# Performance work log

Measured on AMD Instinct MI355X. Metric: run time of the kernel, lower is better.

The kernel has to match this reference:

```python
import jax, jax.numpy as jnp
import numpy as np

W = 0.5  # loss weight from __init__
EPS = 1e-14


def gradient_l2_loss(x):
    """Mean squared forward finite-difference along each spatial axis of (B,s,r,c)."""
    loss = 0.0
    for ax in (1, 2, 3):
        d = jnp.diff(x, axis=ax)
        loss = loss + jnp.mean(d * d)
    return loss


def setup_inputs() -> dict:
    key = jax.random.key(0)
    k1, k2 = jax.random.split(key)
    B, S, R, C = 2, 128, 128, 128
    L = jax.random.normal(k1, (B, 3, S, R, C), dtype=jnp.float32)
    U = jax.random.normal(k2, (B, 9, S, R, C), dtype=jnp.float32)
    return {"L": L, "U": U}


def reference(L, U):
    B, _, S, R, C = U.shape
    # torch.sort(L, dim=1, descending=True) -> indices[:,0] == argmax over the 3 eigenvalues
    idx0 = jnp.argmax(L, axis=1)  # (B,S,R,C) int
    # U channel layout U{row}_{col}: reshape to (B, col=3, row=3, S,R,C)
    Uview = U.reshape(B, 3, 3, S, R, C)
    idx = jnp.broadcast_to(idx0[:, None, None], (B, 3, 1, S, R, C))
    # faithful to original gather(dim=2)[:, :, 0]
    major = jnp.take_along_axis(Uview, idx, axis=2)[:, :, 0]  # (B,3,S,R,C)
    am = jnp.abs(major)
    den = jnp.sum(am * am, axis=1)  # (B,S,R,C)
    den = jnp.where(den < EPS, EPS, den)
    e1, e2, e3 = am[:, 0], am[:, 1], am[:, 2]
    CO = jnp.sqrt(0.5 * ((e1 - e2) ** 2 + (e2 - e3) ** 2 + (e3 - e1) ** 2) / den)
    CO_grad = 0.0
    for i in range(9):  # fixed small channel loop
        CO_grad = CO_grad + gradient_l2_loss(U[:, i])
    return (CO + CO_grad).mean() * W
```

## Files before the change

### kernel.cpp

```cpp
#include <hip/hip_runtime.h>

#define SS 128
#define RR 128
#define CC 128
#define SCH 4
#define EPSF 1e-14f

__global__ __launch_bounds__(256, 4) void scol_main(const float* __restrict__ L,
                                                    const float* __restrict__ U,
                                                    float4* __restrict__ part) {
    const int SRC = SS * RR * CC;
    const int RC  = RR * CC;

    int bid = blockIdx.x;
    int cpx = gridDim.x >> 3;
    int swz = (bid & 7) * cpx + (bid >> 3);

    int rt = swz & 15;
    int sc = (swz >> 4) & 31;
    int b  = swz >> 9;

    int tid = threadIdx.x;
    int c4       = tid & 31;
    int rowLocal = tid >> 5;
    int r  = (rt << 3) + rowLocal;
    int s0 = sc * SCH;
    int c  = c4 << 2;

    bool hr = (r < RR - 1), hc = (c4 < 31);
    float wr = hr ? 1.f : 0.f;
    float wc = hc ? 1.f : 0.f;
    int offr = hr ? CC : 0;

    int pos = (s0 * RR + r) * CC + c;
    const float* Ub = U + (size_t)b * 9 * SRC + pos;
    const float* Lb = L + (size_t)b * 3 * SRC + pos;

    float a_dc = 0.f, a_dr = 0.f, a_ds = 0.f, a_co = 0.f;

    float4 prev[9];
#pragma unroll
    for (int ch = 0; ch < 9; ++ch)
        prev[ch] = *(const float4*)(Ub + ch * SRC);

#pragma unroll 1
    for (int ss = 0; ss < SCH; ++ss) {
        const float* Up = Ub + ss * RC;
        const float* Lp = Lb + ss * RC;

        float4 l0 = *(const float4*)(Lp);
        float4 l1 = *(const float4*)(Lp + SRC);
        float4 l2 = *(const float4*)(Lp + 2 * SRC);
        float L0v[4] = {l0.x, l0.y, l0.z, l0.w};
        float L1v[4] = {l1.x, l1.y, l1.z, l1.w};
        float L2v[4] = {l2.x, l2.y, l2.z, l2.w};
        int idx[4];
#pragma unroll
        for (int j = 0; j < 4; ++j) {
            int id = 0;
            float best = L0v[j];
            if (L1v[j] > best) { best = L1v[j]; id = 1; }
            if (L2v[j] > best) { best = L2v[j]; id = 2; }
            idx[j] = id;
        }

        float am[3][4];
#pragma unroll
        for (int g = 0; g < 3; ++g)
#pragma unroll
            for (int j = 0; j < 4; ++j) am[g][j] = 0.f;

        float t_dcb = 0.f, t_dr = 0.f;

#pragma unroll
        for (int ch = 0; ch < 9; ++ch) {
            float4 uu = *(const float4*)(Up + ch * SRC);
            float4 vr = *(const float4*)(Up + ch * SRC + offr);
            float4 pv = prev[ch];

            int g = ch / 3, m = ch % 3;
            float uuv[4] = {uu.x, uu.y, uu.z, uu.w};
#pragma unroll
            for (int j = 0; j < 4; ++j)
                if (idx[j] == m) am[g][j] = fabsf(uuv[j]);

            float d;
            d = uu.y - uu.x; a_dc += d * d;
            d = uu.z - uu.y; a_dc += d * d;
            d = uu.w - uu.z; a_dc += d * d;
            float un = __shfl_down(uu.x, 1);
            d = un - uu.w; t_dcb += d * d;

            d = vr.x - uu.x; t_dr += d * d;
            d = vr.y - uu.y; t_dr += d * d;
            d = vr.z - uu.z; t_dr += d * d;
            d = vr.w - uu.w; t_dr += d * d;

            d = uu.x - pv.x; a_ds += d * d;
            d = uu.y - pv.y; a_ds += d * d;
            d = uu.z - pv.z; a_ds += d * d;
            d = uu.w - pv.w; a_ds += d * d;

            prev[ch] = uu;
        }
        a_dc += wc * t_dcb;
        a_dr += wr * t_dr;

#pragma unroll
        for (int j = 0; j < 4; ++j) {
            float e1 = am[0][j], e2 = am[1][j], e3 = am[2][j];
            float den = e1 * e1 + e2 * e2 + e3 * e3;
            den = fmaxf(den, EPSF);
            float num = 0.5f * ((e1 - e2) * (e1 - e2) + (e2 - e3) * (e2 - e3) +
                                (e3 - e1) * (e3 - e1));
            a_co += sqrtf(num / den);
        }
    }

    if (s0 + SCH < SS) {
        const float* Up = Ub + SCH * RC;
#pragma unroll
        for (int ch = 0; ch < 9; ++ch) {
            float4 uu = *(const float4*)(Up + ch * SRC);
            float4 pv = prev[ch];
            float d;
            d = uu.x - pv.x; a_ds += d * d;
            d = uu.y - pv.y; a_ds += d * d;
            d = uu.z - pv.z; a_ds += d * d;
            d = uu.w - pv.w; a_ds += d * d;
        }
    }

#pragma unroll
    for (int off = 32; off > 0; off >>= 1) {
        a_co += __shfl_down(a_co, off);
        a_ds += __shfl_down(a_ds, off);
        a_dr += __shfl_down(a_dr, off);
        a_dc += __shfl_down(a_dc, off);
    }

    __shared__ float s_co[4], s_ds[4], s_dr[4], s_dc[4];
    int wid  = threadIdx.x >> 6;
    int lane = threadIdx.x & 63;
    if (lane == 0) {
        s_co[wid] = a_co; s_ds[wid] = a_ds;
        s_dr[wid] = a_dr; s_dc[wid] = a_dc;
    }
    __syncthreads();
    if (threadIdx.x == 0) {
        float t_co = 0.f, t_s = 0.f, t_r = 0.f, t_c = 0.f;
        for (int w = 0; w < 4; ++w) {
            t_co += s_co[w]; t_s += s_ds[w];
            t_r += s_dr[w]; t_c += s_dc[w];
        }
        part[blockIdx.x] = make_float4(t_co, t_s, t_r, t_c);
    }
}

__global__ __launch_bounds__(256) void scol_final(const float4* __restrict__ part,
                                                  float* __restrict__ out,
                                                  int nblk, int B) {
    double d_co = 0., d_ds = 0., d_dr = 0., d_dc = 0.;
    for (int i = threadIdx.x; i < nblk; i += blockDim.x) {
        float4 p = part[i];
        d_co += (double)p.x; d_ds += (double)p.y;
        d_dr += (double)p.z; d_dc += (double)p.w;
    }
#pragma unroll
    for (int off = 32; off > 0; off >>= 1) {
        d_co += __shfl_down(d_co, off);
        d_ds += __shfl_down(d_ds, off);
        d_dr += __shfl_down(d_dr, off);
        d_dc += __shfl_down(d_dc, off);
    }
    __shared__ double sh[4][4];
    int wid  = threadIdx.x >> 6;
    int lane = threadIdx.x & 63;
    if (lane == 0) {
        sh[wid][0] = d_co; sh[wid][1] = d_ds;
        sh[wid][2] = d_dr; sh[wid][3] = d_dc;
    }
    __syncthreads();
    if (threadIdx.x == 0) {
        double t_co = 0., t_ds = 0., t_dr = 0., t_dc = 0.;
        for (int w = 0; w < 4; ++w) {
            t_co += sh[w][0]; t_ds += sh[w][1];
            t_dr += sh[w][2]; t_dc += sh[w][3];
        }
        double nvox = (double)B * SS * RR * CC;
        double nds  = (double)B * (SS - 1) * RR * CC;
        double ndr  = (double)B * SS * (RR - 1) * CC;
        double ndc  = (double)B * SS * RR * (CC - 1);
        out[0] = (float)(0.5 * (t_co / nvox + t_ds / nds + t_dr / ndr + t_dc / ndc));
    }
}

extern "C" void kernel_launch(void* const* d_in, const int* in_sizes, int n_in,
                              void* d_out, int out_size, void* d_ws, size_t ws_size,
                              hipStream_t stream) {
    const float* L = (const float*)d_in[0];
    const float* U = (const float*)d_in[1];
    float* out = (float*)d_out;

    int B = in_sizes[1] / (9 * SS * RR * CC);
    int blocks = B * (SS / SCH) * (RR / 8);

    float4* part = (float4*)d_ws;

    hipLaunchKernelGGL(scol_main, dim3(blocks), dim3(256), 0, stream,
                       L, U, part);
    hipLaunchKernelGGL(scol_final, dim3(1), dim3(256), 0, stream,
                       part, out, blocks, B);
}
```

Before: 250.6 us.

## Split fused kernel into CO gather pass and per-volume gradient streaming pass

```diff
diff --git a/kernel.cpp b/kernel.cpp
--- a/kernel.cpp
+++ b/kernel.cpp
@@ -3,158 +3,181 @@
 #define SS 128
 #define RR 128
 #define CC 128
-#define SCH 4
 #define EPSF 1e-14f
 
-__global__ __launch_bounds__(256, 4) void scol_main(const float* __restrict__ L,
+constexpr int SRC = SS * RR * CC;
+constexpr int RC  = RR * CC;
+
+__global__ __launch_bounds__(256, 4) void co_gather(const float* __restrict__ L,
                                                     const float* __restrict__ U,
                                                     float4* __restrict__ part) {
-    const int SRC = SS * RR * CC;
-    const int RC  = RR * CC;
-
     int bid = blockIdx.x;
     int cpx = gridDim.x >> 3;
     int swz = (bid & 7) * cpx + (bid >> 3);
 
-    int rt = swz & 15;
-    int sc = (swz >> 4) & 31;
-    int b  = swz >> 9;
-
     int tid = threadIdx.x;
-    int c4       = tid & 31;
-    int rowLocal = tid >> 5;
-    int r  = (rt << 3) + rowLocal;
-    int s0 = sc * SCH;
-    int c  = c4 << 2;
+    int c4  = tid & 31;
+    int row = swz * 8 + (tid >> 5);
+    int b   = row >> 14;
+    int c   = c4 << 2;
+
+    int pos    = (row - b * (SS * RR)) * CC + c;
+    const float* Lb = L + (size_t)b * 3 * SRC + pos;
+    const float* Ub = U + (size_t)b * 9 * SRC + pos;
+
+    float4 l0 = *(const float4*)(Lb);
+    float4 l1 = *(const float4*)(Lb + SRC);
+    float4 l2 = *(const float4*)(Lb + 2 * SRC);
+    float4 u[9];
+#pragma unroll
+    for (int ch = 0; ch < 9; ++ch)
+        u[ch] = *(const float4*)(Ub + ch * SRC);
+
+    float L0v[4] = {l0.x, l0.y, l0.z, l0.w};
+    float L1v[4] = {l1.x, l1.y, l1.z, l1.w};
+    float L2v[4] = {l2.x, l2.y, l2.z, l2.w};
+    int idx[4];
+#pragma unroll
+    for (int j = 0; j < 4; ++j) {
+        int id = 0;
+        float best = L0v[j];
+        if (L1v[j] > best) { best = L1v[j]; id = 1; }
+        if (L2v[j] > best) { best = L2v[j]; id = 2; }
+        idx[j] = id;
+    }
+
+    float am[3][4];
+#pragma unroll
+    for (int g = 0; g < 3; ++g)
+#pragma unroll
+        for (int j = 0; j < 4; ++j) am[g][j] = 0.f;
+
+#pragma unroll
+    for (int ch = 0; ch < 9; ++ch) {
+        int g = ch / 3, m = ch % 3;
+        float uuv[4] = {u[ch].x, u[ch].y, u[ch].z, u[ch].w};
+#pragma unroll
+        for (int j = 0; j < 4; ++j)
+            if (idx[j] == m) am[g][j] = fabsf(uuv[j]);
+    }
+
+    float a_co = 0.f;
+#pragma unroll
+    for (int j = 0; j < 4; ++j) {
+        float e1 = am[0][j], e2 = am[1][j], e3 = am[2][j];
+        float den = fmaxf(e1 * e1 + e2 * e2 + e3 * e3, EPSF);
+        float num = 0.5f * ((e1 - e2) * (e1 - e2) + (e2 - e3) * (e2 - e3) +
+                            (e3 - e1) * (e3 - e1));
+        a_co += sqrtf(num / den);
+    }
+
+#pragma unroll
+    for (int off = 32; off > 0; off >>= 1)
+        a_co += __shfl_down(a_co, off);
+
+    __shared__ float s_co[4];
+    int wid  = threadIdx.x >> 6;
+    int lane = threadIdx.x & 63;
+    if (lane == 0) s_co[wid] = a_co;
+    __syncthreads();
+    if (threadIdx.x == 0)
+        part[blockIdx.x] =
+            make_float4(s_co[0] + s_co[1] + s_co[2] + s_co[3], 0.f, 0.f, 0.f);
+}
+
+__global__ __launch_bounds__(256, 4) void grad_stream(const float* __restrict__ U,
+                                                      float4* __restrict__ part) {
+    int bid = blockIdx.x;
+    int cpx = gridDim.x >> 3;
+    int swz = (bid & 7) * cpx + (bid >> 3);
+
+    int rt  = swz & 15;
+    int sc  = (swz >> 4) & 15;
+    int vol = swz >> 8;
+
+    int tid  = threadIdx.x;
+    int c4   = tid & 31;
+    int rowL = tid >> 5;
+    int r    = (rt << 3) + rowL;
+    int s0   = sc << 3;
+    int c    = c4 << 2;
 
     bool hr = (r < RR - 1), hc = (c4 < 31);
     float wr = hr ? 1.f : 0.f;
     float wc = hc ? 1.f : 0.f;
     int offr = hr ? CC : 0;
-
-    int pos = (s0 * RR + r) * CC + c;
-    const float* Ub = U + (size_t)b * 9 * SRC + pos;
-    const float* Lb = L + (size_t)b * 3 * SRC + pos;
-
-    float a_dc = 0.f, a_dr = 0.f, a_ds = 0.f, a_co = 0.f;
-
-    float4 prev[9];
-#pragma unroll
-    for (int ch = 0; ch < 9; ++ch)
-        prev[ch] = *(const float4*)(Ub + ch * SRC);
-
-#pragma unroll 1
-    for (int ss = 0; ss < SCH; ++ss) {
-        const float* Up = Ub + ss * RC;
-        const float* Lp = Lb + ss * RC;
-
-        float4 l0 = *(const float4*)(Lp);
-        float4 l1 = *(const float4*)(Lp + SRC);
-        float4 l2 = *(const float4*)(Lp + 2 * SRC);
-        float L0v[4] = {l0.x, l0.y, l0.z, l0.w};
-        float L1v[4] = {l1.x, l1.y, l1.z, l1.w};
-        float L2v[4] = {l2.x, l2.y, l2.z, l2.w};
-        int idx[4];
-#pragma unroll
-        for (int j = 0; j < 4; ++j) {
-            int id = 0;
-            float best = L0v[j];
-            if (L1v[j] > best) { best = L1v[j]; id = 1; }
-            if (L2v[j] > best) { best = L2v[j]; id = 2; }
-            idx[j] = id;
+    int offb = (s0 + 8 < SS) ? 8 * RC : 7 * RC;
+
+    const float* V = U + (size_t)vol * SRC + ((size_t)s0 * RR + r) * CC + c;
+
+    __shared__ float4 lds[2][8][32];
+
+    float a_ds = 0.f, a_dr = 0.f, a_dc = 0.f;
+
+    float4 cur = *(const float4*)V;
+    float4 prev = cur;
+
+#pragma unroll
+    for (int ss = 0; ss < 8; ++ss) {
+        int no = (ss == 7) ? offb : (ss + 1) * RC;
+        float4 nxt = *(const float4*)(V + no);
+
+        float4 vr7 = cur;
+        if (rowL == 7)
+            vr7 = *(const float4*)(V + ss * RC + offr);
+
+        lds[ss & 1][rowL][c4] = cur;
+        __syncthreads();
+        float4 vr = (rowL < 7) ? lds[ss & 1][rowL + 1][c4] : vr7;
+
+        float d;
+        d = cur.y - cur.x; a_dc += d * d;
+        d = cur.z - cur.y; a_dc += d * d;
+        d = cur.w - cur.z; a_dc += d * d;
+        float un = __shfl_down(cur.x, 1);
+        d = un - cur.w; a_dc += wc * (d * d);
+
+        float tr = 0.f;
+        d = vr.x - cur.x; tr += d * d;
+        d = vr.y - cur.y; tr += d * d;
+        d = vr.z - cur.z; tr += d * d;
+        d = vr.w - cur.w; tr += d * d;
+        a_dr += wr * tr;
+
+        if (ss > 0) {
+            d = cur.x - prev.x; a_ds += d * d;
+            d = cur.y - prev.y; a_ds += d * d;
+            d = cur.z - prev.z; a_ds += d * d;
+            d = cur.w - prev.w; a_ds += d * d;
         }
-
-        float am[3][4];
-#pragma unroll
-        for (int g = 0; g < 3; ++g)
-#pragma unroll
-            for (int j = 0; j < 4; ++j) am[g][j] = 0.f;
-
-        float t_dcb = 0.f, t_dr = 0.f;
-
-#pragma unroll
-        for (int ch = 0; ch < 9; ++ch) {
-            float4 uu = *(const float4*)(Up + ch * SRC);
-            float4 vr = *(const float4*)(Up + ch * SRC + offr);
-            float4 pv = prev[ch];
-
-            int g = ch / 3, m = ch % 3;
-            float uuv[4] = {uu.x, uu.y, uu.z, uu.w};
-#pragma unroll
-            for (int j = 0; j < 4; ++j)
-                if (idx[j] == m) am[g][j] = fabsf(uuv[j]);
-
-            float d;
-            d = uu.y - uu.x; a_dc += d * d;
-            d = uu.z - uu.y; a_dc += d * d;
-            d = uu.w - uu.z; a_dc += d * d;
-            float un = __shfl_down(uu.x, 1);
-            d = un - uu.w; t_dcb += d * d;
-
-            d = vr.x - uu.x; t_dr += d * d;
-            d = vr.y - uu.y; t_dr += d * d;
-            d = vr.z - uu.z; t_dr += d * d;
-            d = vr.w - uu.w; t_dr += d * d;
-
-            d = uu.x - pv.x; a_ds += d * d;
-            d = uu.y - pv.y; a_ds += d * d;
-            d = uu.z - pv.z; a_ds += d * d;
-            d = uu.w - pv.w; a_ds += d * d;
-
-            prev[ch] = uu;
-        }
-        a_dc += wc * t_dcb;
-        a_dr += wr * t_dr;
-
-#pragma unroll
-        for (int j = 0; j < 4; ++j) {
-            float e1 = am[0][j], e2 = am[1][j], e3 = am[2][j];
-            float den = e1 * e1 + e2 * e2 + e3 * e3;
-            den = fmaxf(den, EPSF);
-            float num = 0.5f * ((e1 - e2) * (e1 - e2) + (e2 - e3) * (e2 - e3) +
-                                (e3 - e1) * (e3 - e1));
-            a_co += sqrtf(num / den);
-        }
-    }
-
-    if (s0 + SCH < SS) {
-        const float* Up = Ub + SCH * RC;
-#pragma unroll
-        for (int ch = 0; ch < 9; ++ch) {
-            float4 uu = *(const float4*)(Up + ch * SRC);
-            float4 pv = prev[ch];
-            float d;
-            d = uu.x - pv.x; a_ds += d * d;
-            d = uu.y - pv.y; a_ds += d * d;
-            d = uu.z - pv.z; a_ds += d * d;
-            d = uu.w - pv.w; a_ds += d * d;
-        }
+        prev = cur;
+        cur  = nxt;
+    }
+    {
+        float d;
+        d = cur.x - prev.x; a_ds += d * d;
+        d = cur.y - prev.y; a_ds += d * d;
+        d = cur.z - prev.z; a_ds += d * d;
+        d = cur.w - prev.w; a_ds += d * d;
     }
 
 #pragma unroll
     for (int off = 32; off > 0; off >>= 1) {
-        a_co += __shfl_down(a_co, off);
         a_ds += __shfl_down(a_ds, off);
         a_dr += __shfl_down(a_dr, off);
         a_dc += __shfl_down(a_dc, off);
     }
 
-    __shared__ float s_co[4], s_ds[4], s_dr[4], s_dc[4];
+    __shared__ float s_ds[4], s_dr[4], s_dc[4];
     int wid  = threadIdx.x >> 6;
     int lane = threadIdx.x & 63;
-    if (lane == 0) {
-        s_co[wid] = a_co; s_ds[wid] = a_ds;
-        s_dr[wid] = a_dr; s_dc[wid] = a_dc;
-    }
+    if (lane == 0) { s_ds[wid] = a_ds; s_dr[wid] = a_dr; s_dc[wid] = a_dc; }
     __syncthreads();
-    if (threadIdx.x == 0) {
-        float t_co = 0.f, t_s = 0.f, t_r = 0.f, t_c = 0.f;
-        for (int w = 0; w < 4; ++w) {
-            t_co += s_co[w]; t_s += s_ds[w];
-            t_r += s_dr[w]; t_c += s_dc[w];
-        }
-        part[blockIdx.x] = make_float4(t_co, t_s, t_r, t_c);
-    }
+    if (threadIdx.x == 0)
+        part[blockIdx.x] = make_float4(0.f,
+                                       s_ds[0] + s_ds[1] + s_ds[2] + s_ds[3],
+                                       s_dr[0] + s_dr[1] + s_dr[2] + s_dr[3],
+                                       s_dc[0] + s_dc[1] + s_dc[2] + s_dc[3]);
 }
 
 __global__ __launch_bounds__(256) void scol_final(const float4* __restrict__ part,
@@ -203,12 +226,16 @@
     float* out = (float*)d_out;
 
     int B = in_sizes[1] / (9 * SS * RR * CC);
-    int blocks = B * (SS / SCH) * (RR / 8);
+    int blocks_co   = B * SS * RR / 8;
+    int blocks_grad = B * 9 * 16 * 16;
+    int nblk = blocks_co + blocks_grad;
 
     float4* part = (float4*)d_ws;
 
-    hipLaunchKernelGGL(scol_main, dim3(blocks), dim3(256), 0, stream,
+    hipLaunchKernelGGL(co_gather, dim3(blocks_co), dim3(256), 0, stream,
                        L, U, part);
+    hipLaunchKernelGGL(grad_stream, dim3(blocks_grad), dim3(256), 0, stream,
+                       U, part + blocks_co);
     hipLaunchKernelGGL(scol_final, dim3(1), dim3(256), 0, stream,
-                       part, out, blocks, B);
-}
+                       part, out, nblk, B);
+}
```

Result: slower. 279.5 us (+11.6%).
